# Performance work log

Hardware: AMD Instinct MI355X
Metric: run time of the kernel (lower is better)

The kernel has to match this reference:

```python
import jax, jax.numpy as jnp
import numpy as np
from jax import lax

B, IN_C, H, W = 2, 256, 80, 80
OUT_C = 256
INTER = IN_C // 16          # 16
C4 = IN_C // 4              # 64
K = 3
DIL = [7, 5, 2, 1]
PADS = [(K + (K - 1) * (d - 1)) // 2 for d in DIL]  # same-padding per module formula


def conv2d(x, w, b=None, pad=0, dil=1, groups=1):
    out = lax.conv_general_dilated(
        x, w, (1, 1), [(pad, pad), (pad, pad)], rhs_dilation=(dil, dil),
        dimension_numbers=('NCHW', 'OIHW', 'NCHW'), feature_group_count=groups)
    if b is not None:
        out = out + b[None, :, None, None]
    return out


def bnorm(x, g, b, eps=1e-3):
    # BatchNorm2d in training mode (fresh module): biased batch stats, eps=0.001
    m = x.mean((0, 2, 3), keepdims=True)
    v = x.var((0, 2, 3), keepdims=True)
    return (x - m) * lax.rsqrt(v + eps) * g[None, :, None, None] + b[None, :, None, None]


def gnorm(x, g, b, groups=4, eps=1e-5):
    Bb, C, Hh, Ww = x.shape
    xr = x.reshape(Bb, groups, C // groups, Hh, Ww)
    m = xr.mean((2, 3, 4), keepdims=True)
    v = xr.var((2, 3, 4), keepdims=True)
    xr = (xr - m) * lax.rsqrt(v + eps)
    return xr.reshape(Bb, C, Hh, Ww) * g[None, :, None, None] + b[None, :, None, None]


def setup_inputs() -> dict:
    keys = jax.random.split(jax.random.key(0), 40)

    def w_init(k, shape):
        fan = float(np.prod(shape[1:]))
        return jax.random.normal(k, shape, jnp.float32) / np.sqrt(fan)

    d = {}
    d['z'] = jax.random.normal(keys[0], (B, IN_C, H, W), jnp.float32)
    for i in range(4):  # depthwise dilated convs: (C4, 1, 3, 3)
        d[f'w_at{i}'] = w_init(keys[1 + 2 * i], (C4, 1, K, K))
        d[f'b_at{i}'] = jax.random.normal(keys[2 + 2 * i], (C4,), jnp.float32) * 0.02
    d['gn_w'] = 1.0 + 0.05 * jax.random.normal(keys[9], (IN_C,), jnp.float32)
    d['gn_b'] = 0.05 * jax.random.normal(keys[10], (IN_C,), jnp.float32)
    d['conv_w'] = w_init(keys[11], (IN_C, IN_C, 1, 1))
    d['conv_b'] = jax.random.normal(keys[12], (IN_C,), jnp.float32) * 0.02
    d['c5a_w'] = w_init(keys[13], (INTER, IN_C, 3, 3))
    d['bn5a_w'] = 1.0 + 0.05 * jax.random.normal(keys[14], (INTER,), jnp.float32)
    d['bn5a_b'] = 0.05 * jax.random.normal(keys[15], (INTER,), jnp.float32)
    d['c5c_w'] = w_init(keys[16], (INTER, IN_C, 3, 3))
    d['bn5c_w'] = 1.0 + 0.05 * jax.random.normal(keys[17], (INTER,), jnp.float32)
    d['bn5c_b'] = 0.05 * jax.random.normal(keys[18], (INTER,), jnp.float32)
    d['pq_w'] = w_init(keys[19], (INTER // 8, INTER, 1, 1))
    d['pq_b'] = jax.random.normal(keys[20], (INTER // 8,), jnp.float32) * 0.02
    d['pk_w'] = w_init(keys[21], (INTER // 8, INTER, 1, 1))
    d['pk_b'] = jax.random.normal(keys[22], (INTER // 8,), jnp.float32) * 0.02
    d['pv_w'] = w_init(keys[23], (INTER, INTER, 1, 1))
    d['pv_b'] = jax.random.normal(keys[24], (INTER,), jnp.float32) * 0.02
    d['pa_gamma'] = 0.5 * jnp.ones((1,), jnp.float32)  # nonzero so attn path is exercised
    d['ca_gamma'] = 0.5 * jnp.ones((1,), jnp.float32)
    d['c5b_w'] = w_init(keys[25], (INTER, INTER, 3, 3))
    d['bn5b_w'] = 1.0 + 0.05 * jax.random.normal(keys[26], (INTER,), jnp.float32)
    d['bn5b_b'] = 0.05 * jax.random.normal(keys[27], (INTER,), jnp.float32)
    d['c5d_w'] = w_init(keys[28], (INTER, INTER, 3, 3))
    d['bn5d_w'] = 1.0 + 0.05 * jax.random.normal(keys[29], (INTER,), jnp.float32)
    d['bn5d_b'] = 0.05 * jax.random.normal(keys[30], (INTER,), jnp.float32)
    d['c6_w'] = w_init(keys[31], (OUT_C, INTER, 1, 1))
    d['c6_b'] = jax.random.normal(keys[32], (OUT_C,), jnp.float32) * 0.02
    return d


def reference(z, w_at0, b_at0, w_at1, b_at1, w_at2, b_at2, w_at3, b_at3,
              gn_w, gn_b, conv_w, conv_b,
              c5a_w, bn5a_w, bn5a_b, c5c_w, bn5c_w, bn5c_b,
              pq_w, pq_b, pk_w, pk_b, pv_w, pv_b, pa_gamma, ca_gamma,
              c5b_w, bn5b_w, bn5b_b, c5d_w, bn5d_w, bn5d_b, c6_w, c6_b):
    parts = jnp.split(z, 4, axis=1)
    ws = [w_at0, w_at1, w_at2, w_at3]
    bs = [b_at0, b_at1, b_at2, b_at3]
    zs = [conv2d(parts[i], ws[i], bs[i], pad=PADS[i], dil=DIL[i], groups=C4)
          for i in range(4)]
    zc = jnp.concatenate(zs, axis=1)
    zc = jax.nn.gelu(conv2d(gnorm(zc, gn_w, gn_b), conv_w, conv_b), approximate=False)

    # --- DABlock ---
    feat1 = jax.nn.relu(bnorm(conv2d(zc, c5a_w, pad=1), bn5a_w, bn5a_b))
    Bb, C, Hh, Ww = feat1.shape
    N = Hh * Ww
    # PAM: full HWxHW attention
    q = conv2d(feat1, pq_w, pq_b).reshape(Bb, -1, N)   # (B, C//8, N)
    k = conv2d(feat1, pk_w, pk_b).reshape(Bb, -1, N)
    v = conv2d(feat1, pv_w, pv_b).reshape(Bb, C, N)
    energy = jnp.einsum('bcn,bcm->bnm', q, k)          # (B, N, N)
    att = jax.nn.softmax(energy, axis=-1)
    pa = jnp.einsum('bcm,bnm->bcn', v, att).reshape(Bb, C, Hh, Ww)
    pa = pa_gamma * pa + feat1
    pa_conv = jax.nn.relu(bnorm(conv2d(pa, c5b_w, pad=1), bn5b_w, bn5b_b))

    feat2 = jax.nn.relu(bnorm(conv2d(zc, c5c_w, pad=1), bn5c_w, bn5c_b))
    # CAM: CxC attention
    xf = feat2.reshape(Bb, C, N)
    e = jnp.einsum('bcn,bdn->bcd', xf, xf)             # (B, C, C)
    e = e.max(-1, keepdims=True) - e
    att_c = jax.nn.softmax(e, axis=-1)
    ca = jnp.einsum('bcd,bdn->bcn', att_c, xf).reshape(Bb, C, Hh, Ww)
    ca = ca_gamma * ca + feat2
    ca_conv = jax.nn.relu(bnorm(conv2d(ca, c5d_w, pad=1), bn5d_w, bn5d_b))

    # Dropout2d(p=0.05) is identity in eval mode
    out = jax.nn.relu(conv2d(pa_conv + ca_conv, c6_w, c6_b))
    return out
```

## Files before the change

kernel.cpp:

```cpp
#include <hip/hip_runtime.h>
#include <math.h>

#define HW 6400

typedef __attribute__((ext_vector_type(8))) short bf16x8;
typedef __attribute__((ext_vector_type(4))) float f32x4;

__device__ __forceinline__ float wredsum(float v){
  #pragma unroll
  for (int o = 32; o; o >>= 1) v += __shfl_xor(v, o);
  return v;
}

__device__ __forceinline__ unsigned short f2bf(float f){
  unsigned int u = __float_as_uint(f);
  u += 0x7FFF + ((u >> 16) & 1);
  return (unsigned short)(u >> 16);
}

__device__ __forceinline__ float bf2f(unsigned short s){
  return __uint_as_float((unsigned int)s << 16);
}

__device__ __forceinline__ unsigned int cvt_pk_bf16(float lo, float hi){
  unsigned int r;
  asm("v_cvt_pk_bf16_f32 %0, %1, %2" : "=v"(r) : "v"(lo), "v"(hi));
  return r;
}

__device__ __forceinline__ float gelu(float v){
  return 0.5f * v * (1.f + erff(v * 0.70710678118f));
}

__global__ __launch_bounds__(256) void k_prep(
    const float* __restrict__ wa, const float* __restrict__ wc,
    const float* __restrict__ wb, const float* __restrict__ wd,
    const float* __restrict__ cw, const float* __restrict__ gn_sc,
    const float* __restrict__ cb,
    unsigned short* __restrict__ wbbf,
    unsigned short* __restrict__ cwbf, float* __restrict__ cbp,
    unsigned short* __restrict__ wbbf2){
  int bx = blockIdx.x;
  int tid = threadIdx.x;
  if (bx < 288){
    int i = bx * 256 + tid;
    if (i < 73728){
      int j = i & 7, l = (i >> 3) & 63, f = (i >> 9) & 1, ss = i >> 10;
      int k = ss * 32 + (l >> 4) * 8 + j;
      int off = k >> 8, ic = k & 255;
      int oc = f * 16 + (l & 15);
      float v = (oc < 16) ? wa[(oc * 256 + ic) * 9 + off]
                          : wc[((oc - 16) * 256 + ic) * 9 + off];
      wbbf[i] = f2bf(v);
    }
  } else if (bx < 800){
    int i = (bx - 288) * 256 + tid;
    int b = i >> 16, r = i & 65535;
    int j = r & 7, l = (r >> 3) & 63, f = (r >> 9) & 15, ss = r >> 13;
    int ic = ss * 32 + (l >> 4) * 8 + j;
    int oc = f * 16 + (l & 15);
    cwbf[i] = f2bf(cw[oc * 256 + ic] * gn_sc[(b * 256 + ic) * 2]);
  } else if (bx < 832){
    int bb = bx - 800;
    int b = bb >> 4;
    int oc = (bb & 15) * 16 + (tid >> 4);
    int cp = tid & 15;
    float s2 = 0.f;
    #pragma unroll
    for (int k = 0; k < 16; k++){
      int c = cp * 16 + k;
      s2 += cw[oc * 256 + c] * gn_sc[(b * 256 + c) * 2 + 1];
    }
    s2 += __shfl_xor(s2, 1); s2 += __shfl_xor(s2, 2);
    s2 += __shfl_xor(s2, 4); s2 += __shfl_xor(s2, 8);
    if (cp == 0) cbp[b * 256 + oc] = cb[oc] + s2;
  } else {
    int i = (bx - 832) * 256 + tid;
    if (i < 9216){
      int j = i & 7, l = (i >> 3) & 63, f = (i >> 9) & 1, off = i >> 10;
      int kk = (l >> 4) * 8 + j;
      int oc = f * 16 + (l & 15);
      float v = 0.f;
      if (oc < 16 && kk < 16)        v = wb[(oc * 16 + kk) * 9 + off];
      else if (oc >= 16 && kk >= 16) v = wd[((oc - 16) * 16 + (kk - 16)) * 9 + off];
      wbbf2[i] = f2bf(v);
    }
  }
}

__global__ __launch_bounds__(256) void k_dwt(
    const float* __restrict__ z,
    const float* __restrict__ w0, const float* __restrict__ b0,
    const float* __restrict__ w1, const float* __restrict__ b1,
    const float* __restrict__ w2, const float* __restrict__ b2,
    const float* __restrict__ w3, const float* __restrict__ b3,
    unsigned short* __restrict__ zbf, float* __restrict__ gnpart){
  __shared__ unsigned short lt[64][66];
  int tid = threadIdx.x;
  int g = blockIdx.y, b = blockIdx.z;
  int p0 = blockIdx.x * 64;
  int lane = tid & 63, s = tid >> 6;
  int pix = p0 + lane;
  int h = pix / 80, w = pix % 80;
  const float* wp; const float* bp; int d;
  if (g == 0){ wp = w0; bp = b0; d = 7; }
  else if (g == 1){ wp = w1; bp = b1; d = 5; }
  else if (g == 2){ wp = w2; bp = b2; d = 2; }
  else            { wp = w3; bp = b3; d = 1; }
  int offr[9]; float msk[9];
  #pragma unroll
  for (int kh = 0; kh < 3; kh++){
    #pragma unroll
    for (int kw = 0; kw < 3; kw++){
      bool ok = ((unsigned)(h + (kh - 1) * d) < 80u) && ((unsigned)(w + (kw - 1) * d) < 80u);
      offr[kh * 3 + kw] = ok ? ((kh - 1) * d * 80 + (kw - 1) * d) : 0;
      msk[kh * 3 + kw] = ok ? 1.f : 0.f;
    }
  }
  const float* zb = z + (size_t)(b * 256 + g * 64) * HW + pix;
  for (int j = 0; j < 16; j++){
    int cl = s * 16 + j;
    const float* zin = zb + (size_t)cl * HW;
    const float* wr = wp + cl * 9;
    float acc = bp[cl];
    #pragma unroll
    for (int k = 0; k < 9; k++) acc = fmaf(wr[k], zin[offr[k]] * msk[k], acc);
    float S = wredsum(acc), Q = wredsum(acc * acc);
    if (lane == 0){
      int cg = b * 256 + g * 64 + cl;
      gnpart[(cg * 100 + blockIdx.x) * 2]     = S;
      gnpart[(cg * 100 + blockIdx.x) * 2 + 1] = Q;
    }
    lt[lane][cl] = f2bf(acc);
  }
  __syncthreads();
  int pr = tid >> 2, q = tid & 3;
  const unsigned short* src = &lt[pr][q * 16];
  unsigned int tmp[8];
  #pragma unroll
  for (int u = 0; u < 8; u++) tmp[u] = *(const unsigned int*)(src + u * 2);
  uint4 v0 = make_uint4(tmp[0], tmp[1], tmp[2], tmp[3]);
  uint4 v1 = make_uint4(tmp[4], tmp[5], tmp[6], tmp[7]);
  unsigned short* dst = zbf + ((size_t)b * HW + p0 + pr) * 256 + g * 64 + q * 16;
  *(uint4*)dst = v0;
  *(uint4*)(dst + 8) = v1;
}

__global__ __launch_bounds__(256) void k_gnfin(
    const float* __restrict__ gnpart, const float* __restrict__ gn_w,
    const float* __restrict__ gn_b, float* __restrict__ gn_sc){
  int tid = threadIdx.x; int bg = blockIdx.x;
  int b = bg >> 2, g = bg & 3;
  size_t base = (size_t)(b * 256 + g * 64) * 200;
  float S = 0.f, Q = 0.f;
  for (int i = tid; i < 6400; i += 256){
    S += gnpart[base + 2 * i];
    Q += gnpart[base + 2 * i + 1];
  }
  S = wredsum(S); Q = wredsum(Q);
  __shared__ float l[8];
  int lane = tid & 63, wid = tid >> 6;
  if (lane == 0){ l[wid] = S; l[4 + wid] = Q; }
  __syncthreads();
  float SS = l[0] + l[1] + l[2] + l[3];
  float QQ = l[4] + l[5] + l[6] + l[7];
  float M = 64.f * HW;
  float mean = SS / M;
  float var = QQ / M - mean * mean;
  float rstd = rsqrtf(var + 1e-5f);
  if (tid < 64){
    int c = g * 64 + tid;
    float sc = gn_w[c] * rstd;
    float sh = gn_b[c] - mean * sc;
    gn_sc[(b * 256 + c) * 2] = sc;
    gn_sc[(b * 256 + c) * 2 + 1] = sh;
  }
}

__global__ __launch_bounds__(256) void k_conv1_mfma(
    const unsigned short* __restrict__ zbf,
    const unsigned short* __restrict__ cwbf,
    const float* __restrict__ cbp,
    unsigned short* __restrict__ zbfT){
  __shared__ __align__(16) unsigned char lmem[64 * 512];
  unsigned short* lda = (unsigned short*)lmem;
  unsigned short* lout = (unsigned short*)lmem;
  int tid = threadIdx.x;
  int p0 = blockIdx.x * 64, ocg = blockIdx.y, b = blockIdx.z;
  #pragma unroll
  for (int k = 0; k < 8; k++){
    int m = tid + k * 256;
    int i = m >> 5, c = m & 31;
    bf16x8 val = *(const bf16x8*)(zbf + ((size_t)b * HW + p0 + i) * 256 + c * 8);
    *(bf16x8*)(lda + i * 256 + (c ^ (i & 7)) * 8) = val;
  }
  __syncthreads();
  int wv = tid >> 6, l = tid & 63;
  int row = l & 15, kg = l >> 4;
  int i = wv * 16 + row;
  f32x4 acc0 = {0.f,0.f,0.f,0.f}, acc1 = {0.f,0.f,0.f,0.f};
  f32x4 acc2 = {0.f,0.f,0.f,0.f}, acc3 = {0.f,0.f,0.f,0.f};
  const unsigned short* wp = cwbf + (size_t)b * 65536 + (ocg * 4) * 512 + l * 8;
  #pragma unroll
  for (int s = 0; s < 8; s++){
    int c = s * 4 + kg;
    bf16x8 a = *(const bf16x8*)(lda + i * 256 + (c ^ (i & 7)) * 8);
    const unsigned short* wps = wp + s * 8192;
    bf16x8 b0 = *(const bf16x8*)(wps);
    bf16x8 b1 = *(const bf16x8*)(wps + 512);
    bf16x8 b2 = *(const bf16x8*)(wps + 1024);
    bf16x8 b3 = *(const bf16x8*)(wps + 1536);
    acc0 = __builtin_amdgcn_mfma_f32_16x16x32_bf16(a, b0, acc0, 0, 0, 0);
    acc1 = __builtin_amdgcn_mfma_f32_16x16x32_bf16(a, b1, acc1, 0, 0, 0);
    acc2 = __builtin_amdgcn_mfma_f32_16x16x32_bf16(a, b2, acc2, 0, 0, 0);
    acc3 = __builtin_amdgcn_mfma_f32_16x16x32_bf16(a, b3, acc3, 0, 0, 0);
  }
  __syncthreads();
  const float* cbb = cbp + b * 256 + ocg * 64;
  int oc_l = l & 15;
  int pl = wv * 16 + kg * 4;
  float bs0 = cbb[oc_l], bs1 = cbb[16 + oc_l], bs2 = cbb[32 + oc_l], bs3 = cbb[48 + oc_l];
  #pragma unroll
  for (int r = 0; r < 4; r++){
    lout[(pl + r) * 72 + oc_l]      = f2bf(gelu(acc0[r] + bs0));
    lout[(pl + r) * 72 + 16 + oc_l] = f2bf(gelu(acc1[r] + bs1));
    lout[(pl + r) * 72 + 32 + oc_l] = f2bf(gelu(acc2[r] + bs2));
    lout[(pl + r) * 72 + 48 + oc_l] = f2bf(gelu(acc3[r] + bs3));
  }
  __syncthreads();
  int pix = tid >> 2, q = tid & 3;
  unsigned short* dst = zbfT + ((size_t)b * HW + p0 + pix) * 256 + ocg * 64 + q * 16;
  const unsigned short* src = lout + pix * 72 + q * 16;
  *(uint4*)dst       = *(const uint4*)src;
  *(uint4*)(dst + 8) = *(const uint4*)(src + 8);
}

__device__ __forceinline__ void c5_gload(bf16x8* r, const unsigned short* zbase,
    int p0, int irow, int c31, const int* hh, const int* ww, int off){
  int dy = off / 3 - 1, dx = off % 3 - 1;
  int doff = dy * 80 + dx;
  #pragma unroll
  for (int k = 0; k < 8; k++){
    int op = p0 + irow + k * 8;
    bool v = ((unsigned)(hh[k] + dy) < 80u) && ((unsigned)(ww[k] + dx) < 80u);
    int sp = v ? (op + doff) : op;
    bf16x8 val = *(const bf16x8*)(zbase + (size_t)sp * 256 + c31 * 8);
    if (!v) val = (bf16x8){0, 0, 0, 0, 0, 0, 0, 0};
    r[k] = val;
  }
}

__global__ __launch_bounds__(256) void k_conv5ac2(
    const unsigned short* __restrict__ zbfT,
    const unsigned short* __restrict__ wbbf,
    float* __restrict__ fpre, float* __restrict__ bnpart){
  __shared__ __align__(16) unsigned short lda[2][64 * 256];
  int tid = threadIdx.x;
  int och = blockIdx.y, b = blockIdx.z;
  int p0 = blockIdx.x * 64;
  int irow = tid >> 5, c31 = tid & 31;
  int hh[8], ww[8];
  #pragma unroll
  for (int k = 0; k < 8; k++){
    int op = p0 + irow + k * 8;
    hh[k] = op / 80; ww[k] = op % 80;
  }
  const unsigned short* zbase = zbfT + (size_t)b * HW * 256;
  bf16x8 r[8];
  c5_gload(r, zbase, p0, irow, c31, hh, ww, 0);
  #pragma unroll
  for (int k = 0; k < 8; k++){
    int i = irow + k * 8;
    *(bf16x8*)(lda[0] + i * 256 + (c31 ^ (i & 7)) * 8) = r[k];
  }
  c5_gload(r, zbase, p0, irow, c31, hh, ww, 1);
  int wv = tid >> 6, l = tid & 63;
  int lrow = l & 15, kg = l >> 4;
  int li = wv * 16 + lrow;
  f32x4 acc = {0.f, 0.f, 0.f, 0.f};
  for (int off = 0; off < 9; off++){
    __syncthreads();
    int buf = off & 1;
    const unsigned short* wp = wbbf + (size_t)off * 8192 + och * 512 + l * 8;
    #pragma unroll
    for (int s = 0; s < 8; s++){
      int cc = s * 4 + kg;
      bf16x8 a = *(const bf16x8*)(lda[buf] + li * 256 + (cc ^ (li & 7)) * 8);
      bf16x8 bb = *(const bf16x8*)(wp + s * 1024);
      acc = __builtin_amdgcn_mfma_f32_16x16x32_bf16(a, bb, acc, 0, 0, 0);
    }
    if (off + 1 < 9){
      #pragma unroll
      for (int k = 0; k < 8; k++){
        int i = irow + k * 8;
        *(bf16x8*)(lda[buf ^ 1] + i * 256 + (c31 ^ (i & 7)) * 8) = r[k];
      }
      if (off + 2 < 9) c5_gload(r, zbase, p0, irow, c31, hh, ww, off + 2);
    }
  }
  __syncthreads();
  float* lout = (float*)lda;
  int ocl = l & 15;
  int pl = wv * 16 + kg * 4;
  #pragma unroll
  for (int rr = 0; rr < 4; rr++) lout[ocl * 68 + pl + rr] = acc[rr];
  __syncthreads();
  int oc = tid >> 4, px = (tid & 15) * 4;
  float4 v = *(float4*)(lout + oc * 68 + px);
  *(float4*)(fpre + ((size_t)(b * 32 + och * 16 + oc)) * HW + p0 + px) = v;
  float S = v.x + v.y + v.z + v.w;
  float Q = v.x * v.x + v.y * v.y + v.z * v.z + v.w * v.w;
  #pragma unroll
  for (int o2 = 1; o2 < 16; o2 <<= 1){ S += __shfl_xor(S, o2); Q += __shfl_xor(Q, o2); }
  if ((tid & 15) == 0){
    int ocg = och * 16 + oc;
    bnpart[ocg * 400 + (b * 100 + blockIdx.x) * 2]     = S;
    bnpart[ocg * 400 + (b * 100 + blockIdx.x) * 2 + 1] = Q;
  }
}

__global__ __launch_bounds__(256) void k_featqkv(
    const float* __restrict__ fpre, const float* __restrict__ bnpart,
    const float* __restrict__ w1, const float* __restrict__ b1,
    const float* __restrict__ w2, const float* __restrict__ b2,
    const float* __restrict__ pqw, const float* __restrict__ pqb,
    const float* __restrict__ pkw, const float* __restrict__ pkb,
    const float* __restrict__ pvw, const float* __restrict__ pvb,
    float* __restrict__ feat, float* __restrict__ qkvT){
  __shared__ float lS[8][32], lQ[8][32], lsc[64];
  int tid = threadIdx.x; int b = blockIdx.y;
  {
    int oc = tid & 31, sl = tid >> 5;
    float S = 0.f, Q = 0.f;
    for (int i = sl; i < 200; i += 8){
      S += bnpart[oc * 400 + i * 2];
      Q += bnpart[oc * 400 + i * 2 + 1];
    }
    lS[sl][oc] = S; lQ[sl][oc] = Q;
    __syncthreads();
    if (tid < 32){
      float SS = 0.f, QQ = 0.f;
      #pragma unroll
      for (int s = 0; s < 8; s++){ SS += lS[s][tid]; QQ += lQ[s][tid]; }
      float M = 2.f * HW;
      float mean = SS / M, var = QQ / M - mean * mean;
      float rstd = rsqrtf(var + 1e-3f);
      float w  = (tid < 16) ? w1[tid] : w2[tid - 16];
      float bb = (tid < 16) ? b1[tid] : b2[tid - 16];
      float sc = w * rstd;
      lsc[tid * 2] = sc; lsc[tid * 2 + 1] = bb - mean * sc;
    }
    __syncthreads();
  }
  int n = blockIdx.x * 256 + tid;
  float f1[16], f2[16];
  #pragma unroll
  for (int c = 0; c < 16; c++){
    float v1 = fpre[(b * 32 + c) * HW + n] * lsc[c * 2] + lsc[c * 2 + 1];
    f1[c] = fmaxf(v1, 0.f);
    float v2 = fpre[(b * 32 + 16 + c) * HW + n] * lsc[(16 + c) * 2] + lsc[(16 + c) * 2 + 1];
    f2[c] = fmaxf(v2, 0.f);
    feat[(b * 32 + c) * HW + n] = f1[c];
    feat[(b * 32 + 16 + c) * HW + n] = f2[c];
  }
  float* o = qkvT + ((size_t)b * HW + n) * 20;
  #pragma unroll
  for (int j = 0; j < 2; j++){
    float q = pqb[j], k = pkb[j];
    #pragma unroll
    for (int c = 0; c < 16; c++){ q += pqw[j * 16 + c] * f1[c]; k += pkw[j * 16 + c] * f1[c]; }
    o[j] = q; o[2 + j] = k;
  }
  #pragma unroll
  for (int j = 0; j < 16; j++){
    float v = pvb[j];
    #pragma unroll
    for (int c = 0; c < 16; c++) v += pvw[j * 16 + c] * f1[c];
    o[4 + j] = v;
  }
}

__global__ __launch_bounds__(256) void k_pam_a(
    const float* __restrict__ qkvT, float* __restrict__ part){
  __shared__ __align__(16) float lk0[800];
  __shared__ __align__(16) float lk1[800];
  __shared__ __align__(16) unsigned short lvb[16][808];
  __shared__ float lred[4];
  int tid = threadIdx.x;
  int mc = blockIdx.y, b = blockIdx.z;
  float sqm = 0.f;
  for (int m = tid; m < 800; m += 256){
    const float* kv = qkvT + ((size_t)b * HW + mc * 800 + m) * 20;
    float4 a0 = *(const float4*)kv;
    lk0[m] = a0.z; lk1[m] = a0.w;
    sqm = fmaxf(sqm, a0.z * a0.z + a0.w * a0.w);
    float4 v0 = *(const float4*)(kv + 4);
    float4 v1 = *(const float4*)(kv + 8);
    float4 v2 = *(const float4*)(kv + 12);
    float4 v3 = *(const float4*)(kv + 16);
    lvb[0][m]  = f2bf(v0.x); lvb[1][m]  = f2bf(v0.y);
    lvb[2][m]  = f2bf(v0.z); lvb[3][m]  = f2bf(v0.w);
    lvb[4][m]  = f2bf(v1.x); lvb[5][m]  = f2bf(v1.y);
    lvb[6][m]  = f2bf(v1.z); lvb[7][m]  = f2bf(v1.w);
    lvb[8][m]  = f2bf(v2.x); lvb[9][m]  = f2bf(v2.y);
    lvb[10][m] = f2bf(v2.z); lvb[11][m] = f2bf(v2.w);
    lvb[12][m] = f2bf(v3.x); lvb[13][m] = f2bf(v3.y);
    lvb[14][m] = f2bf(v3.z); lvb[15][m] = f2bf(v3.w);
  }
  #pragma unroll
  for (int o = 32; o; o >>= 1) sqm = fmaxf(sqm, __shfl_xor(sqm, o));
  int lane = tid & 63, wid = tid >> 6;
  if (lane == 0) lred[wid] = sqm;
  __syncthreads();
  float kmax = sqrtf(fmaxf(fmaxf(lred[0], lred[1]), fmaxf(lred[2], lred[3])));
  int wv = tid >> 6, l = tid & 63;
  int row = l & 15, kg = l >> 4;
  int n = blockIdx.x * 64 + wv * 16 + row;
  const float* qp = qkvT + ((size_t)b * HW + n) * 20;
  float q0 = qp[0], q1 = qp[1];
  float mxr = sqrtf(q0 * q0 + q1 * q1) * kmax;
  f32x4 acc = {0.f, 0.f, 0.f, 0.f};
  float zp = 0.f;
  for (int t = 0; t < 25; t++){
    int m0 = t * 32 + kg * 8;
    float4 k0a = *(const float4*)&lk0[m0];
    float4 k0b = *(const float4*)&lk0[m0 + 4];
    float4 k1a = *(const float4*)&lk1[m0];
    float4 k1b = *(const float4*)&lk1[m0 + 4];
    float p0 = __expf(fmaf(q0, k0a.x, q1 * k1a.x) - mxr);
    float p1 = __expf(fmaf(q0, k0a.y, q1 * k1a.y) - mxr);
    float p2 = __expf(fmaf(q0, k0a.z, q1 * k1a.z) - mxr);
    float p3 = __expf(fmaf(q0, k0a.w, q1 * k1a.w) - mxr);
    float p4 = __expf(fmaf(q0, k0b.x, q1 * k1b.x) - mxr);
    float p5 = __expf(fmaf(q0, k0b.y, q1 * k1b.y) - mxr);
    float p6 = __expf(fmaf(q0, k0b.z, q1 * k1b.z) - mxr);
    float p7 = __expf(fmaf(q0, k0b.w, q1 * k1b.w) - mxr);
    zp += ((p0 + p1) + (p2 + p3)) + ((p4 + p5) + (p6 + p7));
    union { unsigned int u[4]; bf16x8 v; } pk;
    pk.u[0] = cvt_pk_bf16(p0, p1);
    pk.u[1] = cvt_pk_bf16(p2, p3);
    pk.u[2] = cvt_pk_bf16(p4, p5);
    pk.u[3] = cvt_pk_bf16(p6, p7);
    bf16x8 vb = *(const bf16x8*)&lvb[row][m0];
    acc = __builtin_amdgcn_mfma_f32_16x16x32_bf16(pk.v, vb, acc, 0, 0, 0);
  }
  zp += __shfl_xor(zp, 16);
  zp += __shfl_xor(zp, 32);
  float* pp = part + ((size_t)(b * 8 + mc) * 18) * HW;
  if (kg == 0){ pp[n] = mxr; pp[HW + n] = zp; }
  int c = l & 15;
  int nr = blockIdx.x * 64 + wv * 16 + (l >> 4) * 4;
  *(f32x4*)&pp[(size_t)(2 + c) * HW + nr] = acc;
}

__global__ __launch_bounds__(256) void k_cam_gram(
    const float* __restrict__ feat, float* __restrict__ e){
  int tid = threadIdx.x;
  int dd = blockIdx.x, c = blockIdx.y, b = blockIdx.z;
  const float* fc = feat + (b * 32 + 16 + c) * HW;
  const float* fd = feat + (b * 32 + 16 + dd) * HW;
  float S = 0.f;
  for (int i = tid; i < HW; i += 256) S += fc[i] * fd[i];
  S = wredsum(S);
  __shared__ float l[4];
  int lane = tid & 63, wid = tid >> 6;
  if (lane == 0) l[wid] = S;
  __syncthreads();
  if (tid == 0) e[(b * 16 + c) * 16 + dd] = l[0] + l[1] + l[2] + l[3];
}

__global__ __launch_bounds__(256) void k_merge(
    const float* __restrict__ part, const float* __restrict__ feat,
    const float* __restrict__ cam_e,
    const float* __restrict__ pa_g, const float* __restrict__ ca_g,
    unsigned short* __restrict__ mc){
  __shared__ float lsm[8][16];
  int tid = threadIdx.x; int y = blockIdx.y, b = blockIdx.z;
  int n = blockIdx.x * 256 + tid;
  union { unsigned short s[8]; uint4 u; } rowo;
  if (y < 2){
    int c0 = y * 8;
    float mxs[8]; float mx = -1e30f;
    #pragma unroll
    for (int m8 = 0; m8 < 8; m8++){
      mxs[m8] = part[((size_t)(b * 8 + m8) * 18) * HW + n];
      mx = fmaxf(mx, mxs[m8]);
    }
    float Z = 0.f, a[8];
    #pragma unroll
    for (int j = 0; j < 8; j++) a[j] = 0.f;
    #pragma unroll
    for (int m8 = 0; m8 < 8; m8++){
      const float* pp = part + ((size_t)(b * 8 + m8) * 18) * HW + n;
      float r = __expf(mxs[m8] - mx);
      Z += pp[HW] * r;
      #pragma unroll
      for (int j = 0; j < 8; j++) a[j] += pp[(size_t)(2 + c0 + j) * HW] * r;
    }
    float invp = pa_g[0] / Z;
    #pragma unroll
    for (int j = 0; j < 8; j++)
      rowo.s[j] = f2bf(fmaf(a[j], invp, feat[(b * 32 + c0 + j) * HW + n]));
    *(uint4*)(mc + ((size_t)b * HW + n) * 32 + c0) = rowo.u;
  } else {
    int c0 = (y - 2) * 8;
    if (tid < 8){
      const float* rowe = cam_e + (b * 16 + c0 + tid) * 16;
      float rr[16]; float mn = 1e30f;
      #pragma unroll
      for (int d = 0; d < 16; d++){ rr[d] = rowe[d]; mn = fminf(mn, rr[d]); }
      float p[16]; float s = 0.f;
      #pragma unroll
      for (int d = 0; d < 16; d++){ p[d] = __expf(mn - rr[d]); s += p[d]; }
      float inv = ca_g[0] / s;
      #pragma unroll
      for (int d = 0; d < 16; d++) lsm[tid][d] = p[d] * inv;
    }
    __syncthreads();
    float f2[16];
    #pragma unroll
    for (int c = 0; c < 16; c++) f2[c] = feat[(b * 32 + 16 + c) * HW + n];
    #pragma unroll
    for (int j = 0; j < 8; j++){
      float s = 0.f;
      #pragma unroll
      for (int d = 0; d < 16; d++) s = fmaf(lsm[j][d], f2[d], s);
      rowo.s[j] = f2bf(s + f2[c0 + j]);
    }
    *(uint4*)(mc + ((size_t)b * HW + n) * 32 + 16 + c0) = rowo.u;
  }
}

__global__ __launch_bounds__(256) void k_conv5bd_mfma(
    const unsigned short* __restrict__ mc,
    const unsigned short* __restrict__ wbbf2,
    unsigned short* __restrict__ bdb, float* __restrict__ bnpart){
  __shared__ __align__(16) unsigned short lda[9 * 2048];
  __shared__ float lS[8][32], lQ[8][32];
  int tid = threadIdx.x;
  int b = blockIdx.z;
  int p0 = blockIdx.x * 64;
  int i = tid >> 2, q = tid & 3;
  int op = p0 + i;
  int h = op / 80, w = op % 80;
  const unsigned short* mb = mc + (size_t)b * HW * 32;
  #pragma unroll
  for (int off = 0; off < 9; off++){
    int dy = off / 3 - 1, dx = off % 3 - 1;
    bool v = ((unsigned)(h + dy) < 80u) && ((unsigned)(w + dx) < 80u);
    int sp = v ? (op + dy * 80 + dx) : op;
    bf16x8 val = *(const bf16x8*)(mb + (size_t)sp * 32 + q * 8);
    if (!v) val = (bf16x8){0, 0, 0, 0, 0, 0, 0, 0};
    int c8 = ((i & 1) * 4 + q) ^ ((i >> 1) & 7);
    *(bf16x8*)(lda + off * 2048 + (i >> 1) * 64 + c8 * 8) = val;
  }
  __syncthreads();
  int wv = tid >> 6, l = tid & 63;
  int row = l & 15, kg = l >> 4;
  int i2 = wv * 16 + row;
  f32x4 acc0 = {0.f, 0.f, 0.f, 0.f};
  f32x4 acc1 = {0.f, 0.f, 0.f, 0.f};
  #pragma unroll
  for (int off = 0; off < 9; off++){
    int c8 = ((i2 & 1) * 4 + kg) ^ ((i2 >> 1) & 7);
    bf16x8 a = *(const bf16x8*)(lda + off * 2048 + (i2 >> 1) * 64 + c8 * 8);
    bf16x8 b0 = *(const bf16x8*)(wbbf2 + off * 1024 + l * 8);
    bf16x8 b1 = *(const bf16x8*)(wbbf2 + off * 1024 + 512 + l * 8);
    acc0 = __builtin_amdgcn_mfma_f32_16x16x32_bf16(a, b0, acc0, 0, 0, 0);
    acc1 = __builtin_amdgcn_mfma_f32_16x16x32_bf16(a, b1, acc1, 0, 0, 0);
  }
  __syncthreads();
  float* lout = (float*)lda;
  int ocl = l & 15;
  int pl = wv * 16 + kg * 4;
  #pragma unroll
  for (int r = 0; r < 4; r++){
    lout[(pl + r) * 34 + ocl]      = acc0[r];
    lout[(pl + r) * 34 + 16 + ocl] = acc1[r];
  }
  __syncthreads();
  {
    int pix = tid >> 2, qq = tid & 3;
    const float* src = lout + pix * 34 + qq * 8;
    union { unsigned int u[4]; bf16x8 v; } pk;
    pk.u[0] = cvt_pk_bf16(src[0], src[1]);
    pk.u[1] = cvt_pk_bf16(src[2], src[3]);
    pk.u[2] = cvt_pk_bf16(src[4], src[5]);
    pk.u[3] = cvt_pk_bf16(src[6], src[7]);
    *(bf16x8*)(bdb + ((size_t)b * HW + p0 + pix) * 32 + qq * 8) = pk.v;
  }
  {
    int oc = tid & 31, grp = tid >> 5;
    float S = 0.f, Q = 0.f;
    #pragma unroll
    for (int r = 0; r < 8; r++){
      float v = lout[(grp * 8 + r) * 34 + oc];
      S += v; Q += v * v;
    }
    lS[grp][oc] = S; lQ[grp][oc] = Q;
  }
  __syncthreads();
  if (tid < 32){
    float S = 0.f, Q = 0.f;
    #pragma unroll
    for (int g2 = 0; g2 < 8; g2++){ S += lS[g2][tid]; Q += lQ[g2][tid]; }
    bnpart[tid * 400 + (b * 100 + blockIdx.x) * 2]     = S;
    bnpart[tid * 400 + (b * 100 + blockIdx.x) * 2 + 1] = Q;
  }
}

__global__ __launch_bounds__(256) void k_c6(
    const unsigned short* __restrict__ bdb, const float* __restrict__ bnpart,
    const float* __restrict__ w1, const float* __restrict__ b1,
    const float* __restrict__ w2, const float* __restrict__ b2,
    const float* __restrict__ w6, const float* __restrict__ b6,
    float* __restrict__ out){
  __shared__ float lS[8][32], lQ[8][32], lsc[64];
  int tid = threadIdx.x; int og = blockIdx.y * 16, b = blockIdx.z;
  {
    int oc = tid & 31, sl = tid >> 5;
    float S = 0.f, Q = 0.f;
    for (int i = sl; i < 200; i += 8){
      S += bnpart[oc * 400 + i * 2];
      Q += bnpart[oc * 400 + i * 2 + 1];
    }
    lS[sl][oc] = S; lQ[sl][oc] = Q;
    __syncthreads();
    if (tid < 32){
      float SS = 0.f, QQ = 0.f;
      #pragma unroll
      for (int s = 0; s < 8; s++){ SS += lS[s][tid]; QQ += lQ[s][tid]; }
      float M = 2.f * HW;
      float mean = SS / M, var = QQ / M - mean * mean;
      float rstd = rsqrtf(var + 1e-3f);
      float w  = (tid < 16) ? w1[tid] : w2[tid - 16];
      float bb = (tid < 16) ? b1[tid] : b2[tid - 16];
      float sc = w * rstd;
      lsc[tid * 2] = sc; lsc[tid * 2 + 1] = bb - mean * sc;
    }
    __syncthreads();
  }
  int n = blockIdx.x * 256 + tid;
  const unsigned short* rowp = bdb + ((size_t)b * HW + n) * 32;
  union { bf16x8 v[4]; unsigned short s[32]; } r;
  r.v[0] = *(const bf16x8*)(rowp);
  r.v[1] = *(const bf16x8*)(rowp + 8);
  r.v[2] = *(const bf16x8*)(rowp + 16);
  r.v[3] = *(const bf16x8*)(rowp + 24);
  float x[16];
  #pragma unroll
  for (int c = 0; c < 16; c++){
    float v1 = bf2f((unsigned short)r.s[c]) * lsc[c * 2] + lsc[c * 2 + 1];
    float v2 = bf2f((unsigned short)r.s[16 + c]) * lsc[(16 + c) * 2] + lsc[(16 + c) * 2 + 1];
    x[c] = fmaxf(v1, 0.f) + fmaxf(v2, 0.f);
  }
  #pragma unroll
  for (int o = 0; o < 16; o++){
    float a = b6[og + o];
    #pragma unroll
    for (int c = 0; c < 16; c++) a += w6[(og + o) * 16 + c] * x[c];
    out[(b * 256 + og + o) * HW + n] = fmaxf(a, 0.f);
  }
}

extern "C" void kernel_launch(void* const* d_in, const int* in_sizes, int n_in,
                              void* d_out, int out_size, void* d_ws, size_t ws_size,
                              hipStream_t stream){
  const float* z      = (const float*)d_in[0];
  const float* w_at0  = (const float*)d_in[1];
  const float* b_at0  = (const float*)d_in[2];
  const float* w_at1  = (const float*)d_in[3];
  const float* b_at1  = (const float*)d_in[4];
  const float* w_at2  = (const float*)d_in[5];
  const float* b_at2  = (const float*)d_in[6];
  const float* w_at3  = (const float*)d_in[7];
  const float* b_at3  = (const float*)d_in[8];
  const float* gn_w   = (const float*)d_in[9];
  const float* gn_b   = (const float*)d_in[10];
  const float* conv_w = (const float*)d_in[11];
  const float* conv_b = (const float*)d_in[12];
  const float* c5a_w  = (const float*)d_in[13];
  const float* bn5a_w = (const float*)d_in[14];
  const float* bn5a_b = (const float*)d_in[15];
  const float* c5c_w  = (const float*)d_in[16];
  const float* bn5c_w = (const float*)d_in[17];
  const float* bn5c_b = (const float*)d_in[18];
  const float* pq_w   = (const float*)d_in[19];
  const float* pq_b   = (const float*)d_in[20];
  const float* pk_w   = (const float*)d_in[21];
  const float* pk_b   = (const float*)d_in[22];
  const float* pv_w   = (const float*)d_in[23];
  const float* pv_b   = (const float*)d_in[24];
  const float* pa_g   = (const float*)d_in[25];
  const float* ca_g   = (const float*)d_in[26];
  const float* c5b_w  = (const float*)d_in[27];
  const float* bn5b_w = (const float*)d_in[28];
  const float* bn5b_b = (const float*)d_in[29];
  const float* c5d_w  = (const float*)d_in[30];
  const float* bn5d_w = (const float*)d_in[31];
  const float* bn5d_b = (const float*)d_in[32];
  const float* c6_w   = (const float*)d_in[33];
  const float* c6_b   = (const float*)d_in[34];

  float* ws = (float*)d_ws;
  unsigned short* ZBF    = (unsigned short*)ws;
  unsigned short* ZC2BFT = (unsigned short*)(ws + 1638400);
  unsigned short* CWBF   = (unsigned short*)(ws + 3276800);
  float* CBP     = ws + 3407872;
  float* FPRE    = ws + 3408384;
  float* FEAT    = FPRE + 409600;
  float* QKVT    = FEAT + 409600;
  unsigned short* MC  = (unsigned short*)(QKVT + 256000);
  unsigned short* BDB = (unsigned short*)(QKVT + 256000 + 204800);
  float* ST      = QKVT + 256000 + 409600;
  float* GN_SC    = ST;
  float* CAM_E    = ST + 1024;
  float* GN_PART  = ST + 2176;
  float* BNA_PART = ST + 104576;
  float* BNB_PART = ST + 117376;
  unsigned short* WBBF  = (unsigned short*)(ST + 130176);
  unsigned short* WBBF2 = (unsigned short*)(ST + 167040);
  float* PART = ws;

  k_dwt<<<dim3(100, 4, 2), 256, 0, stream>>>(z, w_at0, b_at0, w_at1, b_at1,
                                             w_at2, b_at2, w_at3, b_at3, ZBF, GN_PART);
  k_gnfin<<<8, 256, 0, stream>>>(GN_PART, gn_w, gn_b, GN_SC);
  k_prep<<<868, 256, 0, stream>>>(c5a_w, c5c_w, c5b_w, c5d_w, conv_w, GN_SC, conv_b,
                                  WBBF, CWBF, CBP, WBBF2);
  k_conv1_mfma<<<dim3(100, 4, 2), 256, 0, stream>>>(ZBF, CWBF, CBP, ZC2BFT);
  k_conv5ac2<<<dim3(100, 2, 2), 256, 0, stream>>>(ZC2BFT, WBBF, FPRE, BNA_PART);
  k_featqkv<<<dim3(25, 2), 256, 0, stream>>>(FPRE, BNA_PART, bn5a_w, bn5a_b,
                                             bn5c_w, bn5c_b, pq_w, pq_b, pk_w, pk_b,
                                             pv_w, pv_b, FEAT, QKVT);
  k_pam_a<<<dim3(100, 8, 2), 256, 0, stream>>>(QKVT, PART);
  k_cam_gram<<<dim3(16, 16, 2), 256, 0, stream>>>(FEAT, CAM_E);
  k_merge<<<dim3(25, 4, 2), 256, 0, stream>>>(PART, FEAT, CAM_E, pa_g, ca_g, MC);
  k_conv5bd_mfma<<<dim3(100, 1, 2), 256, 0, stream>>>(MC, WBBF2, BDB, BNB_PART);
  k_c6<<<dim3(25, 16, 2), 256, 0, stream>>>(BDB, BNB_PART, bn5b_w, bn5b_b,
                                            bn5d_w, bn5d_b, c6_w, c6_b, (float*)d_out);
}
```

Baseline: 135.6 us.

## Fuse CAM Gram computation into featqkv kernel with per-block partials

Removes the separate k_cam_gram kernel, which re-read the feature maps from global memory with one block per (c,d) pair. k_featqkv now stages the feat2 tile in shared memory and computes a 16x16 partial Gram per block. k_merge sums the 25 partials before its channel softmax. This saves a launch and the redundant global reads, at the cost of extra shared memory and a serial 256-step loop inside k_featqkv, which has only 50 blocks.

```diff
diff --git a/kernel.cpp b/kernel.cpp
--- a/kernel.cpp
+++ b/kernel.cpp
@@ -326,8 +326,10 @@
     const float* __restrict__ pqw, const float* __restrict__ pqb,
     const float* __restrict__ pkw, const float* __restrict__ pkb,
     const float* __restrict__ pvw, const float* __restrict__ pvb,
-    float* __restrict__ feat, float* __restrict__ qkvT){
+    float* __restrict__ feat, float* __restrict__ qkvT,
+    float* __restrict__ cam_part){
   __shared__ float lS[8][32], lQ[8][32], lsc[64];
+  __shared__ float lf2[256][17];
   int tid = threadIdx.x; int b = blockIdx.y;
   {
     int oc = tid & 31, sl = tid >> 5;
@@ -362,6 +364,7 @@
     f2[c] = fmaxf(v2, 0.f);
     feat[(b * 32 + c) * HW + n] = f1[c];
     feat[(b * 32 + 16 + c) * HW + n] = f2[c];
+    lf2[tid][c] = f2[c];
   }
   float* o = qkvT + ((size_t)b * HW + n) * 20;
   #pragma unroll
@@ -378,6 +381,12 @@
     for (int c = 0; c < 16; c++) v += pvw[j * 16 + c] * f1[c];
     o[4 + j] = v;
   }
+  __syncthreads();
+  int cc = tid >> 4, dd = tid & 15;
+  float s = 0.f;
+  #pragma unroll 4
+  for (int p = 0; p < 256; p++) s = fmaf(lf2[p][cc], lf2[p][dd], s);
+  cam_part[((size_t)blockIdx.x * 2 + b) * 256 + tid] = s;
 }
 
 __global__ __launch_bounds__(256) void k_pam_a(
@@ -453,27 +462,12 @@
   *(f32x4*)&pp[(size_t)(2 + c) * HW + nr] = acc;
 }
 
-__global__ __launch_bounds__(256) void k_cam_gram(
-    const float* __restrict__ feat, float* __restrict__ e){
-  int tid = threadIdx.x;
-  int dd = blockIdx.x, c = blockIdx.y, b = blockIdx.z;
-  const float* fc = feat + (b * 32 + 16 + c) * HW;
-  const float* fd = feat + (b * 32 + 16 + dd) * HW;
-  float S = 0.f;
-  for (int i = tid; i < HW; i += 256) S += fc[i] * fd[i];
-  S = wredsum(S);
-  __shared__ float l[4];
-  int lane = tid & 63, wid = tid >> 6;
-  if (lane == 0) l[wid] = S;
-  __syncthreads();
-  if (tid == 0) e[(b * 16 + c) * 16 + dd] = l[0] + l[1] + l[2] + l[3];
-}
-
 __global__ __launch_bounds__(256) void k_merge(
     const float* __restrict__ part, const float* __restrict__ feat,
-    const float* __restrict__ cam_e,
+    const float* __restrict__ cam_part,
     const float* __restrict__ pa_g, const float* __restrict__ ca_g,
     unsigned short* __restrict__ mc){
+  __shared__ float le[256];
   __shared__ float lsm[8][16];
   int tid = threadIdx.x; int y = blockIdx.y, b = blockIdx.z;
   int n = blockIdx.x * 256 + tid;
@@ -504,15 +498,21 @@
     *(uint4*)(mc + ((size_t)b * HW + n) * 32 + c0) = rowo.u;
   } else {
     int c0 = (y - 2) * 8;
+    float s = 0.f;
+    #pragma unroll
+    for (int blk = 0; blk < 25; blk++)
+      s += cam_part[((size_t)blk * 2 + b) * 256 + tid];
+    le[tid] = s;
+    __syncthreads();
     if (tid < 8){
-      const float* rowe = cam_e + (b * 16 + c0 + tid) * 16;
+      int c = c0 + tid;
       float rr[16]; float mn = 1e30f;
       #pragma unroll
-      for (int d = 0; d < 16; d++){ rr[d] = rowe[d]; mn = fminf(mn, rr[d]); }
-      float p[16]; float s = 0.f;
+      for (int d = 0; d < 16; d++){ rr[d] = le[c * 16 + d]; mn = fminf(mn, rr[d]); }
+      float p[16]; float ssum = 0.f;
       #pragma unroll
-      for (int d = 0; d < 16; d++){ p[d] = __expf(mn - rr[d]); s += p[d]; }
-      float inv = ca_g[0] / s;
+      for (int d = 0; d < 16; d++){ p[d] = __expf(mn - rr[d]); ssum += p[d]; }
+      float inv = ca_g[0] / ssum;
       #pragma unroll
       for (int d = 0; d < 16; d++) lsm[tid][d] = p[d] * inv;
     }
@@ -522,10 +522,10 @@
     for (int c = 0; c < 16; c++) f2[c] = feat[(b * 32 + 16 + c) * HW + n];
     #pragma unroll
     for (int j = 0; j < 8; j++){
-      float s = 0.f;
+      float s2 = 0.f;
       #pragma unroll
-      for (int d = 0; d < 16; d++) s = fmaf(lsm[j][d], f2[d], s);
-      rowo.s[j] = f2bf(s + f2[c0 + j]);
+      for (int d = 0; d < 16; d++) s2 = fmaf(lsm[j][d], f2[d], s2);
+      rowo.s[j] = f2bf(s2 + f2[c0 + j]);
     }
     *(uint4*)(mc + ((size_t)b * HW + n) * 32 + 16 + c0) = rowo.u;
   }
@@ -714,12 +714,12 @@
   unsigned short* BDB = (unsigned short*)(QKVT + 256000 + 204800);
   float* ST      = QKVT + 256000 + 409600;
   float* GN_SC    = ST;
-  float* CAM_E    = ST + 1024;
-  float* GN_PART  = ST + 2176;
-  float* BNA_PART = ST + 104576;
-  float* BNB_PART = ST + 117376;
-  unsigned short* WBBF  = (unsigned short*)(ST + 130176);
-  unsigned short* WBBF2 = (unsigned short*)(ST + 167040);
+  float* CAM_PART = ST + 1024;
+  float* GN_PART  = ST + 14336;
+  float* BNA_PART = ST + 116736;
+  float* BNB_PART = ST + 129536;
+  unsigned short* WBBF  = (unsigned short*)(ST + 142336);
+  unsigned short* WBBF2 = (unsigned short*)(ST + 179200);
   float* PART = ws;
 
   k_dwt<<<dim3(100, 4, 2), 256, 0, stream>>>(z, w_at0, b_at0, w_at1, b_at1,
@@ -731,10 +731,9 @@
   k_conv5ac2<<<dim3(100, 2, 2), 256, 0, stream>>>(ZC2BFT, WBBF, FPRE, BNA_PART);
   k_featqkv<<<dim3(25, 2), 256, 0, stream>>>(FPRE, BNA_PART, bn5a_w, bn5a_b,
                                              bn5c_w, bn5c_b, pq_w, pq_b, pk_w, pk_b,
-                                             pv_w, pv_b, FEAT, QKVT);
+                                             pv_w, pv_b, FEAT, QKVT, CAM_PART);
   k_pam_a<<<dim3(100, 8, 2), 256, 0, stream>>>(QKVT, PART);
-  k_cam_gram<<<dim3(16, 16, 2), 256, 0, stream>>>(FEAT, CAM_E);
-  k_merge<<<dim3(25, 4, 2), 256, 0, stream>>>(PART, FEAT, CAM_E, pa_g, ca_g, MC);
+  k_merge<<<dim3(25, 4, 2), 256, 0, stream>>>(PART, FEAT, CAM_PART, pa_g, ca_g, MC);
   k_conv5bd_mfma<<<dim3(100, 1, 2), 256, 0, stream>>>(MC, WBBF2, BDB, BNB_PART);
   k_c6<<<dim3(25, 16, 2), 256, 0, stream>>>(BDB, BNB_PART, bn5b_w, bn5b_b,
                                             bn5d_w, bn5d_b, c6_w, c6_b, (float*)d_out);
```

New measurement: 127.8 us. 1.06x faster.
